# Kernel tuning notes

Hardware: AMD Instinct MI355X
Metric: run time of the kernel (lower is better)

The kernel has to match this reference:

```python
import jax, jax.numpy as jnp
import numpy as np
from jax.scipy.ndimage import map_coordinates

IMG = 256
N_ANG = 50
BATCH = 4
N_CNN = 32
IN_CH = 2


def _circle_mask(S):
    c = (S - 1) / 2.0
    yy, xx = jnp.meshgrid(jnp.arange(S, dtype=jnp.float32), jnp.arange(S, dtype=jnp.float32), indexing='ij')
    return (((yy - c) ** 2 + (xx - c) ** 2) <= (S / 2.0) ** 2).astype(jnp.float32)


def radon_forward(img, angles):
    # img [B,1,S,S] -> sinogram [B,1,A,S]; parallel-beam, clip_to_circle=True
    S = img.shape[-1]
    c = (S - 1) / 2.0
    img = img * _circle_mask(S)
    t = jnp.arange(S, dtype=jnp.float32) - c        # integration coord
    s = jnp.arange(S, dtype=jnp.float32) - c        # detector coord
    cos = jnp.cos(angles)[:, None, None]
    sin = jnp.sin(angles)[:, None, None]
    x = s[None, None, :] * cos - t[None, :, None] * sin   # [A,S,S]
    y = s[None, None, :] * sin + t[None, :, None] * cos
    coords = jnp.stack([y + c, x + c])                    # [2,A,S,S] (row, col)
    samp = jax.vmap(lambda im: map_coordinates(im, coords, order=1, mode='constant', cval=0.0))(img[:, 0])  # [B,A,S,S]
    return samp.sum(axis=2)[:, None]                      # sum over ray param -> [B,1,A,S]


def filter_sinogram(sino):
    # Ram-Lak FFT filter with zero-padding + FBP normalization
    S = sino.shape[-1]
    A = sino.shape[2]
    P = max(64, int(2 ** np.ceil(np.log2(2 * S))))
    f = jnp.fft.rfft(jnp.pad(sino, ((0, 0), (0, 0), (0, 0), (0, P - S))), axis=-1)
    ramp = 2.0 * jnp.fft.rfftfreq(P).astype(jnp.float32)
    out = jnp.fft.irfft(f * ramp, n=P, axis=-1)[..., :S]
    return out * (np.pi / (2.0 * A))


def radon_backprojection(sino, angles):
    # sino [B,1,A,S] -> image [B,1,S,S]
    B, _, A, S = sino.shape
    c = (S - 1) / 2.0
    yy, xx = jnp.meshgrid(jnp.arange(S, dtype=jnp.float32) - c, jnp.arange(S, dtype=jnp.float32) - c, indexing='ij')
    cos = jnp.cos(angles)[:, None, None]
    sin = jnp.sin(angles)[:, None, None]
    det = xx[None] * cos + yy[None] * sin + c             # [A,S,S] detector coord
    sino2 = sino[:, 0]                                    # [B,A,S]

    def interp_one(sino_a, idx):
        # sino_a [B,S], idx [S,S] -> [B,S,S] linear interp, zero outside
        i0 = jnp.clip(jnp.floor(idx).astype(jnp.int32), 0, S - 2)
        w = idx - i0
        v = sino_a[:, i0] * (1.0 - w) + sino_a[:, i0 + 1] * w
        valid = (idx >= 0.0) & (idx <= S - 1.0)
        return jnp.where(valid, v, 0.0)

    bp = jax.vmap(interp_one, in_axes=(1, 0))(sino2, det).sum(axis=0)  # [B,S,S]
    return (bp * _circle_mask(S))[:, None]


def conv2d(x, w, b):
    y = jax.lax.conv_general_dilated(x, w, (1, 1), 'SAME', dimension_numbers=('NCHW', 'OIHW', 'NCHW'))
    return y + b[None, :, None, None]


def setup_inputs() -> dict:
    key = jax.random.key(0)
    ks = jax.random.split(key, 10)
    angles = jnp.asarray(np.linspace(0, np.pi, N_ANG, endpoint=False), dtype=jnp.float32)
    return {
        'x_sinogram': jax.random.normal(ks[0], (BATCH, 1, N_ANG, IMG), dtype=jnp.float32),
        'y_img_prev': jax.random.normal(ks[1], (BATCH, 1, IMG, IMG), dtype=jnp.float32),
        'y_img_concat_prev': jax.random.normal(ks[2], (BATCH, 1, IMG, IMG), dtype=jnp.float32),
        'angles': angles,
        'step': jnp.float32(1.0),
        'w1': jax.random.normal(ks[3], (N_CNN, IN_CH, 3, 3), dtype=jnp.float32) * 0.1,
        'b1': jnp.zeros((N_CNN,), dtype=jnp.float32),
        'w2': jax.random.normal(ks[4], (N_CNN, N_CNN, 3, 3), dtype=jnp.float32) * 0.1,
        'b2': jnp.zeros((N_CNN,), dtype=jnp.float32),
        'w3': jax.random.normal(ks[5], (1, N_CNN, 3, 3), dtype=jnp.float32) * 0.1,
        'b3': jnp.zeros((1,), dtype=jnp.float32),
    }


def reference(x_sinogram, y_img_prev, y_img_concat_prev, angles, step, w1, b1, w2, b2, w3, b3):
    Ay = radon_forward(y_img_prev, angles)                 # [B,1,A,S]
    diff = Ay - x_sinogram
    filt = filter_sinogram(diff)
    fbp = radon_backprojection(filt, angles)               # [B,1,S,S]
    y_img_update = y_img_prev + step * fbp
    y_cat = jnp.concatenate([y_img_update, y_img_concat_prev], axis=1)  # [B,2,S,S]
    h = jax.nn.relu(conv2d(y_cat, w1, b1))
    h = jax.nn.relu(conv2d(h, w2, b2))
    y_img = conv2d(h, w3, b3)
    return (y_img, y_img_update)
```

## Files before the change

### kernel.cpp

```cpp
#include <hip/hip_runtime.h>
#include <math.h>

#define IMGS 256
#define NANG 50
#define BATCH 4
#define NCNN 32
#define PIX (IMGS*IMGS)
#define NPIX (BATCH*PIX)

#define PROW 258
#define PPIX (PROW*PROW)
#define PB   (PPIX*NCNN)

#define OFF_COS   0
#define OFF_SIN   64
#define OFF_TAPS  128
#define OFF_PART  640
#define OFF_FILT  51840
#define OFF_YUPD  103040
#define OFF_W2BF  365184
#define OFF_H1P   369792
#define OFF_H2P   4629888

static constexpr double PI_D = 3.14159265358979323846;

typedef unsigned short u16;
typedef unsigned int   u32;
typedef unsigned long long u64;
typedef __bf16 bfrag __attribute__((ext_vector_type(8)));
typedef float  ffrag __attribute__((ext_vector_type(4)));

__device__ __forceinline__ u16 f2bf(float f) {
    u32 u = __float_as_uint(f);
    u += 0x7fffu + ((u >> 16) & 1u);
    return (u16)(u >> 16);
}

__global__ void k_setup(const float* __restrict__ angles,
                        const float* __restrict__ w2, float* __restrict__ ws) {
    int gid = blockIdx.x, tid = threadIdx.x;
    if (gid < 36) {
        int i = gid * 256 + tid;
        if (i < 9216) {
            int t = i >> 10, oc = (i >> 5) & 31, ic = i & 31;
            ((u16*)(ws + OFF_W2BF))[i] = f2bf(w2[(oc * 32 + ic) * 9 + t]);
        }
    } else if (gid < 38) {
        int q = (gid - 36) * 256 + tid;
        if (q < 511) {
            int d = q - 255;
            int n = d < 0 ? -d : d;
            double g;
            if (n == 0) {
                g = 0.5;
            } else {
                double th = PI_D * (double)n / 256.0;
                double S = (256.0 * cos(255.0 * th) - 255.0 * cos(256.0 * th) - 1.0)
                           / (2.0 * (1.0 - cos(th)));
                double sign = (n & 1) ? -1.0 : 1.0;
                g = (sign + S / 128.0) / 512.0;
            }
            ws[OFF_TAPS + q] = (float)(g * PI_D / 100.0);
        }
    } else if (gid == 38) {
        if (tid < NANG) {
            float a = angles[tid];
            ws[OFF_COS + tid] = cosf(a);
            ws[OFF_SIN + tid] = sinf(a);
        }
    } else {
        int idx = (gid - 39) * 256 + tid;
        if (idx < 2 * BATCH * 1028) {
            int tensor = idx / (BATCH * 1028);
            int r = idx % (BATCH * 1028);
            int b = r / 1028, i = r % 1028;
            int y, x;
            if (i < 516) { y = (i < 258) ? 0 : 257; x = i % 258; }
            else         { int j = i - 516; y = 1 + (j >> 1); x = (j & 1) * 257; }
            u16* base = (u16*)(ws + (tensor ? OFF_H2P : OFF_H1P)) + b * PB + (y * PROW + x) * NCNN;
            uint4 z = make_uint4(0, 0, 0, 0);
            uint4* p4 = (uint4*)base;
            p4[0] = z; p4[1] = z; p4[2] = z; p4[3] = z;
        }
    }
}

#define RPITCH_D 131
__global__ __launch_bounds__(512) void k_radon_fwd(const float* __restrict__ yprev,
                                                   float* __restrict__ ws) {
    __shared__ u16 limg[258 * 262];
    __shared__ float spart[512];
    u32* l32 = (u32*)limg;
    int ra = blockIdx.x;
    int a = ra % NANG, b = ra / NANG;
    int tid = threadIdx.x;

    for (int z = tid; z < 772; z += 512) {
        int addr;
        if (z < 258)      addr = z * RPITCH_D;
        else if (z < 516) addr = (z - 258) * RPITCH_D + 129;
        else if (z < 644) addr = (z - 516) + 1;
        else              addr = 257 * RPITCH_D + (z - 644) + 1;
        l32[addr] = 0;
    }
    const float* __restrict__ src = yprev + b * PIX;
    for (int idx = tid; idx < 16384; idx += 512) {
        int r = idx >> 6, c4 = (idx & 63) << 2;
        float4 v = *(const float4*)(src + r * 256 + c4);
        float di = (float)r - 127.5f;
        float rr = di * di;
        float d0 = (float)c4 - 127.5f;
        v.x = (rr + d0 * d0 <= 16384.0f) ? v.x : 0.0f;
        v.y = (rr + (d0 + 1.0f) * (d0 + 1.0f) <= 16384.0f) ? v.y : 0.0f;
        v.z = (rr + (d0 + 2.0f) * (d0 + 2.0f) <= 16384.0f) ? v.z : 0.0f;
        v.w = (rr + (d0 + 3.0f) * (d0 + 3.0f) <= 16384.0f) ? v.w : 0.0f;
        u32 p0 = (u32)f2bf(v.x) | ((u32)f2bf(v.y) << 16);
        u32 p1 = (u32)f2bf(v.z) | ((u32)f2bf(v.w) << 16);
        int dw = (r + 1) * RPITCH_D + (c4 >> 1) + 1;
        l32[dw] = p0; l32[dw + 1] = p1;
    }
    __syncthreads();

    float cs = ws[OFF_COS + a], sn = ws[OFF_SIN + a];
    int s = tid & 255, half = tid >> 8;
    float sc = (float)s - 127.5f;
    float t0c = 128.0f * (float)half - 127.5f;
    float rowv = sc * sn + t0c * cs + 127.5f;
    float colv = sc * cs - t0c * sn + 127.5f;
    float acc = 0.0f;
    #pragma unroll 4
    for (int it = 0; it < 128; ++it) {
        float fr = floorf(rowv), fc = floorf(colv);
        float wr = rowv - fr, wc = colv - fc;
        int i0 = (int)fr, j0 = (int)fc;
        bool valid = (rowv > -1.0f) & (rowv < 256.0f) & (colv > -1.0f) & (colv < 256.0f);
        int i0c = min(max(i0, -1), 255);
        int j0c = min(max(j0, -1), 255);
        int ca = j0c + 2;
        int ka = ca >> 1;
        int sh = (ca & 1) << 4;
        int dw = (i0c + 1) * RPITCH_D + ka;
        u32 A = l32[dw],            C = l32[dw + 1];
        u32 B = l32[dw + RPITCH_D], D = l32[dw + RPITCH_D + 1];
        u32 top = (u32)((((u64)C << 32) | (u64)A) >> sh);
        u32 bot = (u32)((((u64)D << 32) | (u64)B) >> sh);
        float tl = __uint_as_float(top << 16);
        float tr_ = __uint_as_float(top & 0xffff0000u);
        float bl = __uint_as_float(bot << 16);
        float br = __uint_as_float(bot & 0xffff0000u);
        float tv = tl + (tr_ - tl) * wc;
        float bv = bl + (br - bl) * wc;
        float sv = tv + (bv - tv) * wr;
        acc += valid ? sv : 0.0f;
        rowv += cs; colv -= sn;
    }
    spart[tid] = acc;
    __syncthreads();
    if (tid < 256)
        ws[OFF_PART + ra * 256 + tid] = spart[tid] + spart[tid + 256];
}

__global__ void k_filter(const float* __restrict__ xsino, float* __restrict__ ws) {
    __shared__ float srow[256];
    __shared__ float staps[512];
    int r = blockIdx.x, tid = threadIdx.x;
    srow[tid] = ws[OFF_PART + r * 256 + tid] - xsino[r * 256 + tid];
    staps[tid] = ws[OFF_TAPS + tid];
    if (tid < 255) staps[256 + tid] = ws[OFF_TAPS + 256 + tid];
    __syncthreads();
    float acc = 0.0f;
    #pragma unroll 8
    for (int m = 0; m < 256; ++m) acc += srow[m] * staps[tid - m + 255];
    ws[OFF_FILT + r * 256 + tid] = acc;
}

__global__ void k_backproj(const float* __restrict__ yprev, const float* __restrict__ stepp,
                           float* __restrict__ ws, float* __restrict__ dout) {
    __shared__ float sf[NANG * 256];
    __shared__ float scs[NANG], ssn[NANG];
    int b = blockIdx.x >> 8, i = blockIdx.x & 255, j = threadIdx.x;
    for (int idx = threadIdx.x; idx < NANG * 256; idx += 256)
        sf[idx] = ws[OFF_FILT + b * (NANG * 256) + idx];
    if (threadIdx.x < NANG) {
        scs[threadIdx.x] = ws[OFF_COS + threadIdx.x];
        ssn[threadIdx.x] = ws[OFF_SIN + threadIdx.x];
    }
    __syncthreads();
    float yy = (float)i - 127.5f, xx = (float)j - 127.5f;
    float acc = 0.0f;
    #pragma unroll 5
    for (int a = 0; a < NANG; ++a) {
        float idxf = xx * scs[a] + yy * ssn[a] + 127.5f;
        float fl = floorf(idxf);
        int i0 = (int)fl;
        i0 = min(max(i0, 0), 254);
        float w = idxf - (float)i0;
        float v = sf[a * 256 + i0] * (1.0f - w) + sf[a * 256 + i0 + 1] * w;
        acc += (idxf >= 0.0f && idxf <= 255.0f) ? v : 0.0f;
    }
    float m = (xx * xx + yy * yy <= 16384.0f) ? 1.0f : 0.0f;
    int p = b * PIX + i * 256 + j;
    float upd = yprev[p] + stepp[0] * acc * m;
    ws[OFF_YUPD + p] = upd;
    dout[NPIX + p] = upd;
}

__global__ void k_conv1(const float* __restrict__ yconc, const float* __restrict__ w1,
                        const float* __restrict__ b1, float* __restrict__ ws) {
    int p = blockIdx.x * 256 + threadIdx.x;
    int b = p >> 16, rem = p & 65535, y = rem >> 8, x = rem & 255;
    const float* __restrict__ in0 = ws + OFF_YUPD + b * PIX;
    const float* __restrict__ in1 = yconc + b * PIX;
    float v[18];
    #pragma unroll
    for (int ic = 0; ic < 2; ++ic) {
        const float* __restrict__ in = ic ? in1 : in0;
        #pragma unroll
        for (int ky = 0; ky < 3; ++ky)
            #pragma unroll
            for (int kx = 0; kx < 3; ++kx) {
                int yy = y + ky - 1, xx = x + kx - 1;
                v[ic * 9 + ky * 3 + kx] =
                    ((unsigned)yy < 256u && (unsigned)xx < 256u) ? in[yy * 256 + xx] : 0.0f;
            }
    }
    u32 pk[16];
    #pragma unroll
    for (int oc2 = 0; oc2 < 16; ++oc2) {
        float a0 = b1[2 * oc2], a1 = b1[2 * oc2 + 1];
        const float* wp = w1 + (2 * oc2) * 18;
        #pragma unroll
        for (int t = 0; t < 18; ++t) { a0 += v[t] * wp[t]; a1 += v[t] * wp[18 + t]; }
        a0 = fmaxf(a0, 0.0f); a1 = fmaxf(a1, 0.0f);
        pk[oc2] = (u32)f2bf(a0) | ((u32)f2bf(a1) << 16);
    }
    u16* op = (u16*)(ws + OFF_H1P) + b * PB + ((y + 1) * PROW + (x + 1)) * NCNN;
    uint4* o4 = (uint4*)op;
    #pragma unroll
    for (int q = 0; q < 4; ++q)
        o4[q] = make_uint4(pk[4 * q], pk[4 * q + 1], pk[4 * q + 2], pk[4 * q + 3]);
}

__global__ __launch_bounds__(256) void k_conv2(const float* __restrict__ b2,
                                               float* __restrict__ ws) {
    const u16* __restrict__ w2bf = (const u16*)(ws + OFF_W2BF);
    const u16* __restrict__ h1p  = (const u16*)(ws + OFF_H1P);
    u16* __restrict__ h2p        = (u16*)(ws + OFF_H2P);
    int wg = blockIdx.x;
    int b = wg >> 8, y = wg & 255;
    int wave = threadIdx.x >> 6;
    int lane = threadIdx.x & 63;
    int m = lane & 15, quad = lane >> 4;
    const u16* __restrict__ h1b = h1p + b * PB;
    u16* __restrict__ h2b       = h2p + b * PB;

    bfrag Bf[9][2];
    #pragma unroll
    for (int t = 0; t < 9; ++t) {
        const u16* wp = w2bf + t * 1024 + m * 32 + quad * 8;
        Bf[t][0] = *(const bfrag*)(wp);
        Bf[t][1] = *(const bfrag*)(wp + 16 * 32);
    }
    float bias0 = b2[m], bias1 = b2[m + 16];

    #pragma unroll
    for (int it = 0; it < 4; ++it) {
        int xs = wave * 64 + it * 16;
        bfrag Af[9];
        #pragma unroll
        for (int t = 0; t < 9; ++t) {
            int ty = t / 3, tx = t % 3;
            const u16* ap = h1b + ((y + ty) * PROW + xs + m + tx) * NCNN + quad * 8;
            Af[t] = *(const bfrag*)ap;
        }
        ffrag c0 = {0.f, 0.f, 0.f, 0.f}, c1 = {0.f, 0.f, 0.f, 0.f};
        #pragma unroll
        for (int t = 0; t < 9; ++t) {
            c0 = __builtin_amdgcn_mfma_f32_16x16x32_bf16(Af[t], Bf[t][0], c0, 0, 0, 0);
            c1 = __builtin_amdgcn_mfma_f32_16x16x32_bf16(Af[t], Bf[t][1], c1, 0, 0, 0);
        }
        #pragma unroll
        for (int r = 0; r < 4; ++r) {
            int px = xs + quad * 4 + r;
            u16* op = h2b + ((y + 1) * PROW + px + 1) * NCNN;
            op[m]      = f2bf(fmaxf(c0[r] + bias0, 0.0f));
            op[m + 16] = f2bf(fmaxf(c1[r] + bias1, 0.0f));
        }
    }
}

__global__ void k_conv3(const float* __restrict__ w3, const float* __restrict__ b3,
                        const float* __restrict__ ws, float* __restrict__ dout) {
    __shared__ float sw[288];
    int tid = threadIdx.x;
    for (int idx = tid; idx < 288; idx += 256) {
        int t = idx >> 5, ic = idx & 31;
        sw[idx] = w3[ic * 9 + t];
    }
    __syncthreads();
    int p = blockIdx.x * 256 + tid;
    int b = p >> 16, rem = p & 65535, y = rem >> 8, x = rem & 255;
    const u16* __restrict__ h2b = (const u16*)(ws + OFF_H2P) + b * PB;
    float acc = b3[0];
    #pragma unroll
    for (int t = 0; t < 9; ++t) {
        int ty = t / 3, tx = t % 3;
        const uint4* q = (const uint4*)(h2b + ((y + ty) * PROW + x + tx) * NCNN);
        #pragma unroll
        for (int qq = 0; qq < 4; ++qq) {
            uint4 w4 = q[qq];
            u32 wv[4] = {w4.x, w4.y, w4.z, w4.w};
            #pragma unroll
            for (int k = 0; k < 4; ++k) {
                int ch = qq * 8 + k * 2;
                float f0 = __uint_as_float(wv[k] << 16);
                float f1 = __uint_as_float(wv[k] & 0xffff0000u);
                acc += f0 * sw[t * 32 + ch] + f1 * sw[t * 32 + ch + 1];
            }
        }
    }
    dout[p] = acc;
}

extern "C" void kernel_launch(void* const* d_in, const int* in_sizes, int n_in,
                              void* d_out, int out_size, void* d_ws, size_t ws_size,
                              hipStream_t stream) {
    const float* xsino  = (const float*)d_in[0];
    const float* yprev  = (const float*)d_in[1];
    const float* yconc  = (const float*)d_in[2];
    const float* angles = (const float*)d_in[3];
    const float* stepp  = (const float*)d_in[4];
    const float* w1 = (const float*)d_in[5];
    const float* b1 = (const float*)d_in[6];
    const float* w2 = (const float*)d_in[7];
    const float* b2 = (const float*)d_in[8];
    const float* w3 = (const float*)d_in[9];
    const float* b3 = (const float*)d_in[10];
    float* out = (float*)d_out;
    float* ws  = (float*)d_ws;

    k_setup<<<72, 256, 0, stream>>>(angles, w2, ws);
    k_radon_fwd<<<BATCH * NANG, 512, 0, stream>>>(yprev, ws);
    k_filter<<<BATCH * NANG, 256, 0, stream>>>(xsino, ws);
    k_backproj<<<BATCH * IMGS, 256, 0, stream>>>(yprev, stepp, ws, out);
    k_conv1<<<NPIX / 256, 256, 0, stream>>>(yconc, w1, b1, ws);
    k_conv2<<<BATCH * IMGS, 256, 0, stream>>>(b2, ws);
    k_conv3<<<NPIX / 256, 256, 0, stream>>>(w3, b3, ws, out);
}
```

Before: 170.6 us.

## Fuse seven kernels into three with tiled halo recompute and LDS conv2-conv3

The seven launches become three. The first kernel merges setup, the forward Radon projection and the Ram-Lak filter, computing the filter taps and cos/sin per block. The second fuses backprojection with conv1 over 4-row tiles, recomputing one halo row above and below. The third runs the conv2 MFMA into a 6-row shared-memory h2 tile and does conv3 from it, so the h2 tensor no longer goes through global memory. This removes launch overhead and intermediate HBM traffic, at the cost of redundant halo work (6 rows computed for every 4 output rows), heavier shared memory per block with lower occupancy, and only 256 blocks in the two later kernels.

```diff
diff --git a/kernel.cpp b/kernel.cpp
--- a/kernel.cpp
+++ b/kernel.cpp
@@ -12,15 +12,9 @@
 #define PPIX (PROW*PROW)
 #define PB   (PPIX*NCNN)
 
-#define OFF_COS   0
-#define OFF_SIN   64
-#define OFF_TAPS  128
-#define OFF_PART  640
-#define OFF_FILT  51840
-#define OFF_YUPD  103040
-#define OFF_W2BF  365184
-#define OFF_H1P   369792
-#define OFF_H2P   4629888
+#define OFF_FILT  0
+#define OFF_W2BF  51200
+#define OFF_H1P   55808
 
 static constexpr double PI_D = 3.14159265358979323846;
 
@@ -36,64 +30,45 @@
     return (u16)(u >> 16);
 }
 
-__global__ void k_setup(const float* __restrict__ angles,
-                        const float* __restrict__ w2, float* __restrict__ ws) {
-    int gid = blockIdx.x, tid = threadIdx.x;
-    if (gid < 36) {
-        int i = gid * 256 + tid;
+#define RPITCH_D 131
+__global__ __launch_bounds__(512) void k_A(const float* __restrict__ angles,
+                                           const float* __restrict__ yprev,
+                                           const float* __restrict__ xsino,
+                                           const float* __restrict__ w2,
+                                           float* __restrict__ ws) {
+    __shared__ u16 limg[258 * 262];
+    __shared__ float spart[512];
+    __shared__ float staps[512];
+    __shared__ float srow[256];
+    int tid = threadIdx.x;
+    int gid = blockIdx.x;
+    if (gid >= 200) {
+        int i = (gid - 200) * 512 + tid;
         if (i < 9216) {
             int t = i >> 10, oc = (i >> 5) & 31, ic = i & 31;
             ((u16*)(ws + OFF_W2BF))[i] = f2bf(w2[(oc * 32 + ic) * 9 + t]);
         }
-    } else if (gid < 38) {
-        int q = (gid - 36) * 256 + tid;
-        if (q < 511) {
-            int d = q - 255;
-            int n = d < 0 ? -d : d;
-            double g;
-            if (n == 0) {
-                g = 0.5;
-            } else {
-                double th = PI_D * (double)n / 256.0;
-                double S = (256.0 * cos(255.0 * th) - 255.0 * cos(256.0 * th) - 1.0)
-                           / (2.0 * (1.0 - cos(th)));
-                double sign = (n & 1) ? -1.0 : 1.0;
-                g = (sign + S / 128.0) / 512.0;
-            }
-            ws[OFF_TAPS + q] = (float)(g * PI_D / 100.0);
-        }
-    } else if (gid == 38) {
-        if (tid < NANG) {
-            float a = angles[tid];
-            ws[OFF_COS + tid] = cosf(a);
-            ws[OFF_SIN + tid] = sinf(a);
-        }
-    } else {
-        int idx = (gid - 39) * 256 + tid;
-        if (idx < 2 * BATCH * 1028) {
-            int tensor = idx / (BATCH * 1028);
-            int r = idx % (BATCH * 1028);
-            int b = r / 1028, i = r % 1028;
-            int y, x;
-            if (i < 516) { y = (i < 258) ? 0 : 257; x = i % 258; }
-            else         { int j = i - 516; y = 1 + (j >> 1); x = (j & 1) * 257; }
-            u16* base = (u16*)(ws + (tensor ? OFF_H2P : OFF_H1P)) + b * PB + (y * PROW + x) * NCNN;
-            uint4 z = make_uint4(0, 0, 0, 0);
-            uint4* p4 = (uint4*)base;
-            p4[0] = z; p4[1] = z; p4[2] = z; p4[3] = z;
-        }
-    }
-}
-
-#define RPITCH_D 131
-__global__ __launch_bounds__(512) void k_radon_fwd(const float* __restrict__ yprev,
-                                                   float* __restrict__ ws) {
-    __shared__ u16 limg[258 * 262];
-    __shared__ float spart[512];
+        return;
+    }
     u32* l32 = (u32*)limg;
-    int ra = blockIdx.x;
+    int ra = gid;
     int a = ra % NANG, b = ra / NANG;
-    int tid = threadIdx.x;
+
+    if (tid < 511) {
+        int d = tid - 255;
+        int n = d < 0 ? -d : d;
+        double g;
+        if (n == 0) {
+            g = 0.5;
+        } else {
+            double th = PI_D * (double)n / 256.0;
+            double S = (256.0 * cos(255.0 * th) - 255.0 * cos(256.0 * th) - 1.0)
+                       / (2.0 * (1.0 - cos(th)));
+            double sign = (n & 1) ? -1.0 : 1.0;
+            g = (sign + S / 128.0) / 512.0;
+        }
+        staps[tid] = (float)(g * PI_D / 100.0);
+    }
 
     for (int z = tid; z < 772; z += 512) {
         int addr;
@@ -121,7 +96,8 @@
     }
     __syncthreads();
 
-    float cs = ws[OFF_COS + a], sn = ws[OFF_SIN + a];
+    float a_ = angles[a];
+    float cs = cosf(a_), sn = sinf(a_);
     int s = tid & 255, half = tid >> 8;
     float sc = (float)s - 127.5f;
     float t0c = 128.0f * (float)half - 127.5f;
@@ -157,103 +133,154 @@
     spart[tid] = acc;
     __syncthreads();
     if (tid < 256)
-        ws[OFF_PART + ra * 256 + tid] = spart[tid] + spart[tid + 256];
-}
-
-__global__ void k_filter(const float* __restrict__ xsino, float* __restrict__ ws) {
-    __shared__ float srow[256];
-    __shared__ float staps[512];
-    int r = blockIdx.x, tid = threadIdx.x;
-    srow[tid] = ws[OFF_PART + r * 256 + tid] - xsino[r * 256 + tid];
-    staps[tid] = ws[OFF_TAPS + tid];
-    if (tid < 255) staps[256 + tid] = ws[OFF_TAPS + 256 + tid];
-    __syncthreads();
-    float acc = 0.0f;
-    #pragma unroll 8
-    for (int m = 0; m < 256; ++m) acc += srow[m] * staps[tid - m + 255];
-    ws[OFF_FILT + r * 256 + tid] = acc;
-}
-
-__global__ void k_backproj(const float* __restrict__ yprev, const float* __restrict__ stepp,
-                           float* __restrict__ ws, float* __restrict__ dout) {
+        srow[tid] = spart[tid] + spart[tid + 256] - xsino[ra * 256 + tid];
+    __syncthreads();
+    {
+        float fa = 0.0f;
+        int m0 = half * 128;
+        #pragma unroll 8
+        for (int m = m0; m < m0 + 128; ++m) fa += srow[m] * staps[s - m + 255];
+        spart[tid] = fa;
+    }
+    __syncthreads();
+    if (tid < 256)
+        ws[OFF_FILT + ra * 256 + tid] = spart[tid] + spart[tid + 256];
+}
+
+__global__ __launch_bounds__(512) void k_B(const float* __restrict__ angles,
+                                           const float* __restrict__ yprev,
+                                           const float* __restrict__ yconc,
+                                           const float* __restrict__ stepp,
+                                           const float* __restrict__ w1,
+                                           const float* __restrict__ b1,
+                                           float* __restrict__ ws,
+                                           float* __restrict__ dout) {
     __shared__ float sf[NANG * 256];
+    __shared__ float supd[6][258];
     __shared__ float scs[NANG], ssn[NANG];
-    int b = blockIdx.x >> 8, i = blockIdx.x & 255, j = threadIdx.x;
-    for (int idx = threadIdx.x; idx < NANG * 256; idx += 256)
+    int tid = threadIdx.x;
+    int b = blockIdx.x >> 6, tile = blockIdx.x & 63;
+    int y0 = tile << 2;
+
+    for (int idx = tid; idx < NANG * 256; idx += 512)
         sf[idx] = ws[OFF_FILT + b * (NANG * 256) + idx];
-    if (threadIdx.x < NANG) {
-        scs[threadIdx.x] = ws[OFF_COS + threadIdx.x];
-        ssn[threadIdx.x] = ws[OFF_SIN + threadIdx.x];
-    }
-    __syncthreads();
-    float yy = (float)i - 127.5f, xx = (float)j - 127.5f;
-    float acc = 0.0f;
-    #pragma unroll 5
-    for (int a = 0; a < NANG; ++a) {
-        float idxf = xx * scs[a] + yy * ssn[a] + 127.5f;
-        float fl = floorf(idxf);
-        int i0 = (int)fl;
-        i0 = min(max(i0, 0), 254);
-        float w = idxf - (float)i0;
-        float v = sf[a * 256 + i0] * (1.0f - w) + sf[a * 256 + i0 + 1] * w;
-        acc += (idxf >= 0.0f && idxf <= 255.0f) ? v : 0.0f;
-    }
-    float m = (xx * xx + yy * yy <= 16384.0f) ? 1.0f : 0.0f;
-    int p = b * PIX + i * 256 + j;
-    float upd = yprev[p] + stepp[0] * acc * m;
-    ws[OFF_YUPD + p] = upd;
-    dout[NPIX + p] = upd;
-}
-
-__global__ void k_conv1(const float* __restrict__ yconc, const float* __restrict__ w1,
-                        const float* __restrict__ b1, float* __restrict__ ws) {
-    int p = blockIdx.x * 256 + threadIdx.x;
-    int b = p >> 16, rem = p & 65535, y = rem >> 8, x = rem & 255;
-    const float* __restrict__ in0 = ws + OFF_YUPD + b * PIX;
-    const float* __restrict__ in1 = yconc + b * PIX;
-    float v[18];
+    if (tid < NANG) {
+        float a_ = angles[tid];
+        scs[tid] = cosf(a_); ssn[tid] = sinf(a_);
+    }
+    if (tid < 12) supd[tid >> 1][(tid & 1) * 257] = 0.0f;
+    {
+        int px_i0 = tile * 17;
+        if (tid < 272) {
+            int px_i = px_i0 + (tid >> 4), dw = tid & 15;
+            if (px_i < 1028) {
+                int y, x;
+                if (px_i < 516) { y = (px_i < 258) ? 0 : 257; x = px_i % 258; }
+                else            { int j = px_i - 516; y = 1 + (j >> 1); x = (j & 1) * 257; }
+                u32* p = (u32*)((u16*)(ws + OFF_H1P) + b * PB + (y * PROW + x) * NCNN);
+                p[dw] = 0;
+            }
+        }
+    }
+    __syncthreads();
+
+    float step = stepp[0];
+    for (int k = 0; k < 3; ++k) {
+        int px = tid + k * 512;
+        int r = px >> 8, j = px & 255;
+        int iy = y0 - 1 + r;
+        float val = 0.0f;
+        if ((unsigned)iy < 256u) {
+            float yy = (float)iy - 127.5f, xx = (float)j - 127.5f;
+            float acc = 0.0f;
+            #pragma unroll 5
+            for (int a = 0; a < NANG; ++a) {
+                float idxf = xx * scs[a] + yy * ssn[a] + 127.5f;
+                float fl = floorf(idxf);
+                int i0 = (int)fl;
+                i0 = min(max(i0, 0), 254);
+                float w = idxf - (float)i0;
+                float v = sf[a * 256 + i0] * (1.0f - w) + sf[a * 256 + i0 + 1] * w;
+                acc += (idxf >= 0.0f && idxf <= 255.0f) ? v : 0.0f;
+            }
+            float m = (xx * xx + yy * yy <= 16384.0f) ? 1.0f : 0.0f;
+            val = yprev[b * PIX + iy * 256 + j] + step * acc * m;
+            if (r >= 1 && r <= 4)
+                dout[NPIX + b * PIX + iy * 256 + j] = val;
+        }
+        supd[r][j + 1] = val;
+    }
+    __syncthreads();
+
+    for (int k = 0; k < 2; ++k) {
+        int px = tid + k * 512;
+        int rr = px >> 8, x = px & 255;
+        int oy = y0 + rr;
+        float v[18];
+        #pragma unroll
+        for (int ky = 0; ky < 3; ++ky)
+            #pragma unroll
+            for (int kx = 0; kx < 3; ++kx)
+                v[ky * 3 + kx] = supd[rr + ky][x + kx];
+        const float* __restrict__ in1 = yconc + b * PIX;
+        #pragma unroll
+        for (int ky = 0; ky < 3; ++ky)
+            #pragma unroll
+            for (int kx = 0; kx < 3; ++kx) {
+                int yy = oy + ky - 1, xx = x + kx - 1;
+                v[9 + ky * 3 + kx] =
+                    ((unsigned)yy < 256u && (unsigned)xx < 256u) ? in1[yy * 256 + xx] : 0.0f;
+            }
+        u32 pk[16];
+        #pragma unroll
+        for (int oc2 = 0; oc2 < 16; ++oc2) {
+            float a0 = b1[2 * oc2], a1 = b1[2 * oc2 + 1];
+            const float* wp = w1 + (2 * oc2) * 18;
+            #pragma unroll
+            for (int t = 0; t < 18; ++t) { a0 += v[t] * wp[t]; a1 += v[t] * wp[18 + t]; }
+            a0 = fmaxf(a0, 0.0f); a1 = fmaxf(a1, 0.0f);
+            pk[oc2] = (u32)f2bf(a0) | ((u32)f2bf(a1) << 16);
+        }
+        uint4* o4 = (uint4*)((u16*)(ws + OFF_H1P) + b * PB + ((oy + 1) * PROW + (x + 1)) * NCNN);
+        #pragma unroll
+        for (int q = 0; q < 4; ++q)
+            o4[q] = make_uint4(pk[4 * q], pk[4 * q + 1], pk[4 * q + 2], pk[4 * q + 3]);
+    }
+}
+
+#define H2PITCH 34
+__global__ __launch_bounds__(512) void k_C(const float* __restrict__ b2,
+                                           const float* __restrict__ w3,
+                                           const float* __restrict__ b3,
+                                           float* __restrict__ ws,
+                                           float* __restrict__ dout) {
+    __shared__ u16 sh2[6 * 258 * H2PITCH];
+    __shared__ float sw[288];
+    u32* l32 = (u32*)sh2;
+    int tid = threadIdx.x;
+    int b = blockIdx.x >> 6, tile = blockIdx.x & 63;
+    int y0 = tile << 2;
+
+    for (int idx = tid; idx < 288; idx += 512)
+        sw[idx] = w3[(idx & 31) * 9 + (idx >> 5)];
+    for (int idx = tid; idx < 6 * 2 * 17; idx += 512) {
+        int r = idx / 34, rem = idx % 34;
+        int col = (rem < 17) ? 0 : 257, dw = rem % 17;
+        l32[(r * 258 + col) * 17 + dw] = 0;
+    }
     #pragma unroll
-    for (int ic = 0; ic < 2; ++ic) {
-        const float* __restrict__ in = ic ? in1 : in0;
-        #pragma unroll
-        for (int ky = 0; ky < 3; ++ky)
-            #pragma unroll
-            for (int kx = 0; kx < 3; ++kx) {
-                int yy = y + ky - 1, xx = x + kx - 1;
-                v[ic * 9 + ky * 3 + kx] =
-                    ((unsigned)yy < 256u && (unsigned)xx < 256u) ? in[yy * 256 + xx] : 0.0f;
-            }
-    }
-    u32 pk[16];
-    #pragma unroll
-    for (int oc2 = 0; oc2 < 16; ++oc2) {
-        float a0 = b1[2 * oc2], a1 = b1[2 * oc2 + 1];
-        const float* wp = w1 + (2 * oc2) * 18;
-        #pragma unroll
-        for (int t = 0; t < 18; ++t) { a0 += v[t] * wp[t]; a1 += v[t] * wp[18 + t]; }
-        a0 = fmaxf(a0, 0.0f); a1 = fmaxf(a1, 0.0f);
-        pk[oc2] = (u32)f2bf(a0) | ((u32)f2bf(a1) << 16);
-    }
-    u16* op = (u16*)(ws + OFF_H1P) + b * PB + ((y + 1) * PROW + (x + 1)) * NCNN;
-    uint4* o4 = (uint4*)op;
-    #pragma unroll
-    for (int q = 0; q < 4; ++q)
-        o4[q] = make_uint4(pk[4 * q], pk[4 * q + 1], pk[4 * q + 2], pk[4 * q + 3]);
-}
-
-__global__ __launch_bounds__(256) void k_conv2(const float* __restrict__ b2,
-                                               float* __restrict__ ws) {
+    for (int r = 0; r < 6; ++r) {
+        int hy = y0 - 1 + r;
+        if (hy < 0 || hy > 255)
+            for (int idx = tid; idx < 258 * 17; idx += 512)
+                l32[r * 258 * 17 + idx] = 0;
+    }
+    __syncthreads();
+
     const u16* __restrict__ w2bf = (const u16*)(ws + OFF_W2BF);
-    const u16* __restrict__ h1p  = (const u16*)(ws + OFF_H1P);
-    u16* __restrict__ h2p        = (u16*)(ws + OFF_H2P);
-    int wg = blockIdx.x;
-    int b = wg >> 8, y = wg & 255;
-    int wave = threadIdx.x >> 6;
-    int lane = threadIdx.x & 63;
+    const u16* __restrict__ h1b  = (const u16*)(ws + OFF_H1P) + b * PB;
+    int wave = tid >> 6, lane = tid & 63;
     int m = lane & 15, quad = lane >> 4;
-    const u16* __restrict__ h1b = h1p + b * PB;
-    u16* __restrict__ h2b       = h2p + b * PB;
-
     bfrag Bf[9][2];
     #pragma unroll
     for (int t = 0; t < 9; ++t) {
@@ -262,64 +289,68 @@
         Bf[t][1] = *(const bfrag*)(wp + 16 * 32);
     }
     float bias0 = b2[m], bias1 = b2[m + 16];
-
     #pragma unroll
-    for (int it = 0; it < 4; ++it) {
-        int xs = wave * 64 + it * 16;
-        bfrag Af[9];
-        #pragma unroll
-        for (int t = 0; t < 9; ++t) {
-            int ty = t / 3, tx = t % 3;
-            const u16* ap = h1b + ((y + ty) * PROW + xs + m + tx) * NCNN + quad * 8;
-            Af[t] = *(const bfrag*)ap;
-        }
-        ffrag c0 = {0.f, 0.f, 0.f, 0.f}, c1 = {0.f, 0.f, 0.f, 0.f};
-        #pragma unroll
-        for (int t = 0; t < 9; ++t) {
-            c0 = __builtin_amdgcn_mfma_f32_16x16x32_bf16(Af[t], Bf[t][0], c0, 0, 0, 0);
-            c1 = __builtin_amdgcn_mfma_f32_16x16x32_bf16(Af[t], Bf[t][1], c1, 0, 0, 0);
-        }
-        #pragma unroll
-        for (int r = 0; r < 4; ++r) {
-            int px = xs + quad * 4 + r;
-            u16* op = h2b + ((y + 1) * PROW + px + 1) * NCNN;
-            op[m]      = f2bf(fmaxf(c0[r] + bias0, 0.0f));
-            op[m + 16] = f2bf(fmaxf(c1[r] + bias1, 0.0f));
-        }
-    }
-}
-
-__global__ void k_conv3(const float* __restrict__ w3, const float* __restrict__ b3,
-                        const float* __restrict__ ws, float* __restrict__ dout) {
-    __shared__ float sw[288];
-    int tid = threadIdx.x;
-    for (int idx = tid; idx < 288; idx += 256) {
-        int t = idx >> 5, ic = idx & 31;
-        sw[idx] = w3[ic * 9 + t];
-    }
-    __syncthreads();
-    int p = blockIdx.x * 256 + tid;
-    int b = p >> 16, rem = p & 65535, y = rem >> 8, x = rem & 255;
-    const u16* __restrict__ h2b = (const u16*)(ws + OFF_H2P) + b * PB;
-    float acc = b3[0];
-    #pragma unroll
-    for (int t = 0; t < 9; ++t) {
-        int ty = t / 3, tx = t % 3;
-        const uint4* q = (const uint4*)(h2b + ((y + ty) * PROW + x + tx) * NCNN);
-        #pragma unroll
-        for (int qq = 0; qq < 4; ++qq) {
-            uint4 w4 = q[qq];
-            u32 wv[4] = {w4.x, w4.y, w4.z, w4.w};
-            #pragma unroll
-            for (int k = 0; k < 4; ++k) {
-                int ch = qq * 8 + k * 2;
-                float f0 = __uint_as_float(wv[k] << 16);
-                float f1 = __uint_as_float(wv[k] & 0xffff0000u);
-                acc += f0 * sw[t * 32 + ch] + f1 * sw[t * 32 + ch + 1];
-            }
-        }
-    }
-    dout[p] = acc;
+    for (int k = 0; k < 12; ++k) {
+        int tl = wave + (k << 3);
+        int ridx = tl >> 4, xt = tl & 15;
+        int hy = y0 - 1 + ridx;
+        if ((unsigned)hy < 256u) {
+            int xs = xt << 4;
+            bfrag Af[9];
+            #pragma unroll
+            for (int t = 0; t < 9; ++t) {
+                int ty = t / 3, tx = t % 3;
+                const u16* ap = h1b + ((hy + ty) * PROW + xs + m + tx) * NCNN + quad * 8;
+                Af[t] = *(const bfrag*)ap;
+            }
+            ffrag c0 = {0.f, 0.f, 0.f, 0.f}, c1 = {0.f, 0.f, 0.f, 0.f};
+            #pragma unroll
+            for (int t = 0; t < 9; ++t) {
+                c0 = __builtin_amdgcn_mfma_f32_16x16x32_bf16(Af[t], Bf[t][0], c0, 0, 0, 0);
+                c1 = __builtin_amdgcn_mfma_f32_16x16x32_bf16(Af[t], Bf[t][1], c1, 0, 0, 0);
+            }
+            #pragma unroll
+            for (int r = 0; r < 4; ++r) {
+                int px = xs + quad * 4 + r;
+                u16* op = sh2 + (ridx * 258 + px + 1) * H2PITCH;
+                op[m]      = f2bf(fmaxf(c0[r] + bias0, 0.0f));
+                op[m + 16] = f2bf(fmaxf(c1[r] + bias1, 0.0f));
+            }
+        }
+    }
+    __syncthreads();
+
+    {
+        int pid = tid * 2;
+        int rr = pid >> 8, x = pid & 255;
+        int oy = y0 + rr;
+        float bias = b3[0];
+        float a0 = bias, a1 = bias;
+        #pragma unroll
+        for (int ky = 0; ky < 3; ++ky) {
+            #pragma unroll
+            for (int cx = 0; cx < 4; ++cx) {
+                const u32* q = l32 + ((rr + ky) * 258 + x + cx) * 17;
+                #pragma unroll
+                for (int kd = 0; kd < 16; ++kd) {
+                    u32 wv = q[kd];
+                    float f0 = __uint_as_float(wv << 16);
+                    float f1 = __uint_as_float(wv & 0xffff0000u);
+                    int ch = kd * 2;
+                    if (cx < 3) {
+                        int t = ky * 3 + cx;
+                        a0 += f0 * sw[t * 32 + ch] + f1 * sw[t * 32 + ch + 1];
+                    }
+                    if (cx > 0) {
+                        int t = ky * 3 + cx - 1;
+                        a1 += f0 * sw[t * 32 + ch] + f1 * sw[t * 32 + ch + 1];
+                    }
+                }
+            }
+        }
+        float* op = dout + b * PIX + oy * 256 + x;
+        op[0] = a0; op[1] = a1;
+    }
 }
 
 extern "C" void kernel_launch(void* const* d_in, const int* in_sizes, int n_in,
@@ -339,11 +370,7 @@
     float* out = (float*)d_out;
     float* ws  = (float*)d_ws;
 
-    k_setup<<<72, 256, 0, stream>>>(angles, w2, ws);
-    k_radon_fwd<<<BATCH * NANG, 512, 0, stream>>>(yprev, ws);
-    k_filter<<<BATCH * NANG, 256, 0, stream>>>(xsino, ws);
-    k_backproj<<<BATCH * IMGS, 256, 0, stream>>>(yprev, stepp, ws, out);
-    k_conv1<<<NPIX / 256, 256, 0, stream>>>(yconc, w1, b1, ws);
-    k_conv2<<<BATCH * IMGS, 256, 0, stream>>>(b2, ws);
-    k_conv3<<<NPIX / 256, 256, 0, stream>>>(w3, b3, ws, out);
-}
+    k_A<<<218, 512, 0, stream>>>(angles, yprev, xsino, w2, ws);
+    k_B<<<BATCH * 64, 512, 0, stream>>>(angles, yprev, yconc, stepp, w1, b1, ws, out);
+    k_C<<<BATCH * 64, 512, 0, stream>>>(b2, w3, b3, ws, out);
+}
```

New measurement: 172.4 us. Within noise of the previous version (+1.0%).
